# Kernel optimization log

Measured on AMD Instinct MI355X. Metric: run time of the kernel, lower is better.

## Reference

```python
import jax, jax.numpy as jnp
import numpy as np

N_NODES = 100000
N_EDGES = 1600000
D_IN = 128
D_HID = 128
D_OUT = 64


def _glorot(key, shape):
    lim = float(np.sqrt(6.0 / (shape[0] + shape[1])))
    return jax.random.uniform(key, shape, jnp.float32, -lim, lim)


def setup_inputs() -> dict:
    key = jax.random.key(0)
    ks = jax.random.split(key, 8)
    x = jax.random.normal(ks[0], (N_NODES, D_IN), jnp.float32)
    edge_index = jax.random.randint(ks[1], (2, N_EDGES), 0, N_NODES, jnp.int64)
    # SAGEConv layer 0: in=128 -> out=128 (lin_l with bias on aggregated, lin_r no bias on root)
    W_l0 = _glorot(ks[2], (D_IN, D_HID))
    b_l0 = jnp.zeros((D_HID,), jnp.float32)
    W_r0 = _glorot(ks[3], (D_IN, D_HID))
    # SAGEConv layer 1: in=128 -> out=64
    W_l1 = _glorot(ks[4], (D_HID, D_OUT))
    b_l1 = jnp.zeros((D_OUT,), jnp.float32)
    W_r1 = _glorot(ks[5], (D_HID, D_OUT))
    return {"x": x, "edge_index": edge_index,
            "W_l0": W_l0, "b_l0": b_l0, "W_r0": W_r0,
            "W_l1": W_l1, "b_l1": b_l1, "W_r1": W_r1}


def _sage_conv(x, src, dst, W_l, b_l, W_r):
    # mean aggregation of source features at targets (PyG SAGEConv default aggr='mean')
    msgs = x[src]                                              # [E, d_in] irregular gather
    agg = jax.ops.segment_sum(msgs, dst, num_segments=N_NODES)  # [N, d_in]
    cnt = jax.ops.segment_sum(jnp.ones((src.shape[0],), x.dtype), dst,
                              num_segments=N_NODES)            # [N]
    mean = agg / jnp.maximum(cnt, 1.0)[:, None]
    return mean @ W_l + b_l + x @ W_r


def reference(x, edge_index, W_l0, b_l0, W_r0, W_l1, b_l1, W_r1):
    src, dst = edge_index[0], edge_index[1]
    h = _sage_conv(x, src, dst, W_l0, b_l0, W_r0)
    h = jax.nn.relu(h)
    # dropout is identity at inference (training=False)
    out = _sage_conv(h, src, dst, W_l1, b_l1, W_r1)
    return out
```

## Files before the change

### kernel.cpp

```cpp
#include <hip/hip_runtime.h>
#include <type_traits>

#define NN 100000
#define NE 1600000
#define DF 128
#define NBKT 196
#define BKT_SHIFT 9
#define EPB 6250
#define NPB2 391

typedef unsigned short ushort_t;
typedef unsigned int uint_t;
typedef __bf16 bf16x8 __attribute__((ext_vector_type(8)));
typedef float f32x4 __attribute__((ext_vector_type(4)));

union ABFrag { uint4 u; bf16x8 v; ushort_t s[8]; };

__device__ __forceinline__ ushort_t f2bf(float f) {
    uint_t u;
    __builtin_memcpy(&u, &f, 4);
    uint_t rounding = 0x7FFFu + ((u >> 16) & 1u);
    u += rounding;
    return (ushort_t)(u >> 16);
}
__device__ __forceinline__ float lo_f(uint_t u) { return __uint_as_float(u << 16); }
__device__ __forceinline__ float hi_f(uint_t u) { return __uint_as_float(u & 0xffff0000u); }
__device__ __forceinline__ uint_t pack2(float a, float b) {
    return (uint_t)f2bf(a) | ((uint_t)f2bf(b) << 16);
}

__device__ __forceinline__ int detect64(const int* ei, int* s64) {
    if (threadIdx.x < 64) {
        int v = ei[threadIdx.x];
        bool ok = ((threadIdx.x & 1) == 0) || (v == 0);
        unsigned long long m = __ballot(ok);
        if (threadIdx.x == 0) *s64 = (m == 0xFFFFFFFFFFFFFFFFULL) ? 1 : 0;
    }
    __syncthreads();
    return *s64;
}

__global__ __launch_bounds__(256) void k_bktcnt(const int* __restrict__ ei,
                                                int* __restrict__ M) {
    __shared__ int cnt[NBKT];
    __shared__ int s64;
    int t = threadIdx.x, blk = blockIdx.x;
    int is64 = detect64(ei, &s64);
    for (int i = t; i < NBKT; i += 256) cnt[i] = 0;
    __syncthreads();
    int e0 = blk * EPB;
    if (is64) {
        const long long* p = (const long long*)ei;
        for (int i = t; i < EPB; i += 256) {
            int d = (int)p[(size_t)NE + e0 + i];
            atomicAdd(&cnt[d >> BKT_SHIFT], 1);
        }
    } else {
        for (int i = t; i < EPB; i += 256) {
            int d = ei[NE + e0 + i];
            atomicAdd(&cnt[d >> BKT_SHIFT], 1);
        }
    }
    __syncthreads();
    for (int i = t; i < NBKT; i += 256) M[i * 256 + blk] = cnt[i];
}

__global__ __launch_bounds__(256) void k_colscan(int* __restrict__ M, int* __restrict__ colsum) {
    __shared__ int sm[256];
    int t = threadIdx.x, b = blockIdx.x;
    int v = M[b * 256 + t];
    sm[t] = v;
    __syncthreads();
    for (int o = 1; o < 256; o <<= 1) {
        int add = (t >= o) ? sm[t - o] : 0;
        __syncthreads();
        sm[t] += add;
        __syncthreads();
    }
    M[b * 256 + t] = sm[t] - v;
    if (t == 255) colsum[b] = sm[255];
}

__global__ __launch_bounds__(256) void k_bktscan(const int* __restrict__ colsum,
                                                 int* __restrict__ bkbase, int* __restrict__ rs) {
    __shared__ int sm[256];
    int t = threadIdx.x;
    int v = (t < NBKT) ? colsum[t] : 0;
    sm[t] = v;
    __syncthreads();
    for (int o = 1; o < 256; o <<= 1) {
        int add = (t >= o) ? sm[t - o] : 0;
        __syncthreads();
        sm[t] += add;
        __syncthreads();
    }
    if (t <= NBKT) bkbase[t] = sm[t] - v;
    if (t == 0) rs[NN] = NE;
}

__global__ void k_scan512(const int* __restrict__ c2, int* __restrict__ dbase) {
    __shared__ int sm[512];
    int t = threadIdx.x;
    int v = c2[t];
    sm[t] = v;
    __syncthreads();
    for (int o = 1; o < 512; o <<= 1) {
        int add = (t >= o) ? sm[t - o] : 0;
        __syncthreads();
        sm[t] += add;
        __syncthreads();
    }
    dbase[t] = sm[t] - v;
}

__global__ __launch_bounds__(256) void k_bktscatter(const int* __restrict__ ei,
                                                    const int* __restrict__ M,
                                                    const int* __restrict__ bkbase,
                                                    uint2* __restrict__ tmp) {
    __shared__ int cur[NBKT];
    __shared__ int s64;
    int t = threadIdx.x, blk = blockIdx.x;
    int is64 = detect64(ei, &s64);
    for (int i = t; i < NBKT; i += 256) cur[i] = bkbase[i] + M[i * 256 + blk];
    __syncthreads();
    int e0 = blk * EPB;
    if (is64) {
        const long long* p = (const long long*)ei;
        for (int i = t; i < EPB; i += 256) {
            int e = e0 + i;
            int s = (int)p[e], d = (int)p[(size_t)NE + e];
            int pos = atomicAdd(&cur[d >> BKT_SHIFT], 1);
            tmp[pos] = make_uint2((uint_t)s, (uint_t)d);
        }
    } else {
        for (int i = t; i < EPB; i += 256) {
            int e = e0 + i;
            int s = ei[e], d = ei[NE + e];
            int pos = atomicAdd(&cur[d >> BKT_SHIFT], 1);
            tmp[pos] = make_uint2((uint_t)s, (uint_t)d);
        }
    }
}

__global__ __launch_bounds__(256) void k_bktsort(const uint2* __restrict__ tmp,
                                                 const int* __restrict__ bkbase,
                                                 int* __restrict__ rs, int* __restrict__ esrc) {
    __shared__ int hist[512];
    __shared__ int curp[512];
    int t = threadIdx.x, b = blockIdx.x;
    int nbase = b << BKT_SHIFT;
    int bb = bkbase[b], be = bkbase[b + 1];
    hist[t] = 0;
    hist[t + 256] = 0;
    __syncthreads();
    for (int i = bb + t; i < be; i += 256)
        atomicAdd(&hist[(int)tmp[i].y - nbase], 1);
    __syncthreads();
    int ov0 = hist[t], ov1 = hist[t + 256];
    for (int o = 1; o < 512; o <<= 1) {
        int v0 = (t >= o) ? hist[t - o] : 0;
        int v1 = (t + 256 >= o) ? hist[t + 256 - o] : 0;
        __syncthreads();
        hist[t] += v0;
        hist[t + 256] += v1;
        __syncthreads();
    }
    int ex0 = bb + hist[t] - ov0;
    int ex1 = bb + hist[t + 256] - ov1;
    int n0 = nbase + t, n1 = nbase + t + 256;
    if (n0 < NN) rs[n0] = ex0;
    if (n1 < NN) rs[n1] = ex1;
    curp[t] = ex0;
    curp[t + 256] = ex1;
    __syncthreads();
    for (int i = bb + t; i < be; i += 256) {
        uint2 pr = tmp[i];
        int pos = atomicAdd(&curp[(int)pr.y - nbase], 1);
        esrc[pos] = (int)pr.x;
    }
}

__global__ __launch_bounds__(256) void k_dcnt(const int* __restrict__ rs, int* __restrict__ M2) {
    __shared__ int cnt[512];
    int t = threadIdx.x, b = blockIdx.x;
    cnt[t] = 0;
    cnt[t + 256] = 0;
    __syncthreads();
    int base = b * NPB2;
    for (int i = t; i < NPB2; i += 256) {
        int n = base + i;
        if (n < NN) {
            int d = rs[n + 1] - rs[n];
            if (d > 511) d = 511;
            atomicAdd(&cnt[d], 1);
        }
    }
    __syncthreads();
    M2[t * 256 + b] = cnt[t];
    M2[(t + 256) * 256 + b] = cnt[t + 256];
}

__global__ __launch_bounds__(256) void k_dperm(const int* __restrict__ rs,
                                               const int* __restrict__ M2,
                                               const int* __restrict__ dbase,
                                               int* __restrict__ perm) {
    __shared__ int cur[512];
    int t = threadIdx.x, b = blockIdx.x;
    cur[t] = dbase[t] + M2[t * 256 + b];
    cur[t + 256] = dbase[t + 256] + M2[(t + 256) * 256 + b];
    __syncthreads();
    int base = b * NPB2;
    for (int i = t; i < NPB2; i += 256) {
        int n = base + i;
        if (n < NN) {
            int d = rs[n + 1] - rs[n];
            if (d > 511) d = 511;
            int pos = atomicAdd(&cur[d], 1);
            perm[pos] = n;
        }
    }
}

#define CAST_B 12501
__global__ void k_prep(const float* __restrict__ x, ushort_t* __restrict__ xb,
                       const float* __restrict__ Wl0, const float* __restrict__ Wr0,
                       ushort_t* __restrict__ pw0,
                       const float* __restrict__ Wl1, const float* __restrict__ Wr1,
                       ushort_t* __restrict__ pw1) {
    const int n4 = NN * DF / 4;
    int blk = blockIdx.x, t = threadIdx.x;
    if (blk < CAST_B) {
        int i = blk * 256 + t;
        if (i < n4) {
            float4 f = ((const float4*)x)[i];
            uint2 o;
            o.x = pack2(f.x, f.y);
            o.y = pack2(f.z, f.w);
            ((uint2*)xb)[i] = o;
        } else if (i < n4 + 32) {
            ((uint2*)xb)[i] = make_uint2(0u, 0u);
        }
    } else if (blk < CAST_B + 128) {
        int idx = (blk - CAST_B) * 256 + t;
        int j = idx & 7;
        int lane = (idx >> 3) & 63;
        int rem = idx / 512;
        int tt = rem % 8;
        int s = rem / 8;
        int quad = lane >> 4, l16 = lane & 15;
        int k = (s & 3) * 32 + quad * 8 + j;
        int n = tt * 16 + l16;
        const float* W = (s < 4) ? Wl0 : Wr0;
        pw0[idx] = f2bf(W[k * 128 + n]);
    } else {
        int idx = (blk - CAST_B - 128) * 256 + t;
        int j = idx & 7;
        int lane = (idx >> 3) & 63;
        int rem = idx / 512;
        int tt = rem % 8;
        int s = rem / 8;
        int quad = lane >> 4, l16 = lane & 15;
        int k = s * 32 + quad * 8 + j;
        int n = (tt & 3) * 16 + l16;
        const float* W = (tt < 4) ? Wl1 : Wr1;
        pw1[idx] = f2bf(W[k * 64 + n]);
    }
}

__global__ __launch_bounds__(256) void k_agg0(const ushort_t* __restrict__ xb,
                                              const int* __restrict__ rs,
                                              const int* __restrict__ esrc,
                                              const int* __restrict__ perm,
                                              ushort_t* __restrict__ outm) {
    int wv = threadIdx.x >> 6;
    int lane = threadIdx.x & 63;
    int l16 = lane & 15, gbase = lane & 48;
    int slot = (blockIdx.x * 4 + wv) * 4 + (lane >> 4);
    int n = perm[slot];
    int s0 = rs[n];
    int deg = rs[n + 1] - s0;
    if (deg == 0) s0 = 0;
    int md = deg;
    md = max(md, __shfl_xor(md, 16));
    md = max(md, __shfl_xor(md, 32));
    float acc[8] = {0.f, 0.f, 0.f, 0.f, 0.f, 0.f, 0.f, 0.f};
    const ushort_t* fb = xb + l16 * 8;
    int clampIdx = (deg > 0) ? deg - 1 : 0;
    for (int c = 0; c < md; c += 16) {
        int ii = c + l16;
        if (ii > clampIdx) ii = clampIdx;
        int my = esrc[s0 + ii];
        int lim = md - c;
        if (lim > 16) lim = 16;
        int e = 0;
        for (; e + 4 <= lim; e += 4) {
            int r0 = __shfl(my, gbase + e);
            int r1 = __shfl(my, gbase + e + 1);
            int r2 = __shfl(my, gbase + e + 2);
            int r3 = __shfl(my, gbase + e + 3);
            r0 = (c + e < deg) ? r0 : NN;
            r1 = (c + e + 1 < deg) ? r1 : NN;
            r2 = (c + e + 2 < deg) ? r2 : NN;
            r3 = (c + e + 3 < deg) ? r3 : NN;
            uint4 v0 = *(const uint4*)(fb + (size_t)r0 * DF);
            uint4 v1 = *(const uint4*)(fb + (size_t)r1 * DF);
            uint4 v2 = *(const uint4*)(fb + (size_t)r2 * DF);
            uint4 v3 = *(const uint4*)(fb + (size_t)r3 * DF);
            acc[0] += lo_f(v0.x); acc[1] += hi_f(v0.x); acc[2] += lo_f(v0.y); acc[3] += hi_f(v0.y);
            acc[4] += lo_f(v0.z); acc[5] += hi_f(v0.z); acc[6] += lo_f(v0.w); acc[7] += hi_f(v0.w);
            acc[0] += lo_f(v1.x); acc[1] += hi_f(v1.x); acc[2] += lo_f(v1.y); acc[3] += hi_f(v1.y);
            acc[4] += lo_f(v1.z); acc[5] += hi_f(v1.z); acc[6] += lo_f(v1.w); acc[7] += hi_f(v1.w);
            acc[0] += lo_f(v2.x); acc[1] += hi_f(v2.x); acc[2] += lo_f(v2.y); acc[3] += hi_f(v2.y);
            acc[4] += lo_f(v2.z); acc[5] += hi_f(v2.z); acc[6] += lo_f(v2.w); acc[7] += hi_f(v2.w);
            acc[0] += lo_f(v3.x); acc[1] += hi_f(v3.x); acc[2] += lo_f(v3.y); acc[3] += hi_f(v3.y);
            acc[4] += lo_f(v3.z); acc[5] += hi_f(v3.z); acc[6] += lo_f(v3.w); acc[7] += hi_f(v3.w);
        }
        for (; e < lim; ++e) {
            int r = __shfl(my, gbase + e);
            r = (c + e < deg) ? r : NN;
            uint4 v = *(const uint4*)(fb + (size_t)r * DF);
            acc[0] += lo_f(v.x); acc[1] += hi_f(v.x); acc[2] += lo_f(v.y); acc[3] += hi_f(v.y);
            acc[4] += lo_f(v.z); acc[5] += hi_f(v.z); acc[6] += lo_f(v.w); acc[7] += hi_f(v.w);
        }
    }
    float inv = 1.0f / (float)(deg > 0 ? deg : 1);
    uint4 o;
    o.x = pack2(acc[0] * inv, acc[1] * inv);
    o.y = pack2(acc[2] * inv, acc[3] * inv);
    o.z = pack2(acc[4] * inv, acc[5] * inv);
    o.w = pack2(acc[6] * inv, acc[7] * inv);
    *(uint4*)(outm + (size_t)n * DF + l16 * 8) = o;
}

__global__ __launch_bounds__(256) void k_gemmF(const ushort_t* __restrict__ A0,
                                               const ushort_t* __restrict__ A1,
                                               const ushort_t* __restrict__ pw0,
                                               const float* __restrict__ bl0,
                                               const ushort_t* __restrict__ pw1,
                                               const float* __restrict__ bl1,
                                               ushort_t* __restrict__ tbuf,
                                               float* __restrict__ rbuf) {
    __shared__ ushort_t h_lds[64][136];
    int warp = threadIdx.x >> 6;
    int lane = threadIdx.x & 63;
    int quad = lane >> 4;
    int l16 = lane & 15;
    int m0 = blockIdx.x * 64 + warp * 16;

    int rowA = m0 + l16;
    if (rowA >= NN) rowA = NN - 1;
    const int kofs = quad * 8;

    f32x4 acc[8];
#pragma unroll
    for (int t = 0; t < 8; t++) acc[t] = (f32x4){0.f, 0.f, 0.f, 0.f};

#pragma unroll
    for (int s = 0; s < 8; s++) {
        const ushort_t* Ab = (s < 4) ? A0 : A1;
        int kk = (s & 3) * 32 + kofs;
        ABFrag a;
        a.u = *(const uint4*)(Ab + (size_t)rowA * DF + kk);
#pragma unroll
        for (int t = 0; t < 8; t++) {
            ABFrag b;
            b.u = *(const uint4*)(pw0 + ((size_t)(s * 8 + t) * 64 + lane) * 8);
            acc[t] = __builtin_amdgcn_mfma_f32_16x16x32_bf16(a.v, b.v, acc[t], 0, 0, 0);
        }
    }
#pragma unroll
    for (int t = 0; t < 8; t++) {
        int col = t * 16 + l16;
        float bv = bl0[col];
#pragma unroll
        for (int r = 0; r < 4; r++)
            h_lds[warp * 16 + quad * 4 + r][col] = f2bf(fmaxf(acc[t][r] + bv, 0.f));
    }
    __syncthreads();

    f32x4 c1[8];
#pragma unroll
    for (int t = 0; t < 8; t++) c1[t] = (f32x4){0.f, 0.f, 0.f, 0.f};
#pragma unroll
    for (int s = 0; s < 4; s++) {
        ABFrag a;
        a.u = *(const uint4*)&h_lds[warp * 16 + l16][s * 32 + kofs];
#pragma unroll
        for (int t = 0; t < 8; t++) {
            ABFrag b;
            b.u = *(const uint4*)(pw1 + ((size_t)(s * 8 + t) * 64 + lane) * 8);
            c1[t] = __builtin_amdgcn_mfma_f32_16x16x32_bf16(a.v, b.v, c1[t], 0, 0, 0);
        }
    }
#pragma unroll
    for (int t = 0; t < 8; t++) {
        int cc = (t & 3) * 16 + l16;
        if (t < 4) {
#pragma unroll
            for (int r = 0; r < 4; r++) {
                int row = m0 + quad * 4 + r;
                if (row < NN) tbuf[(size_t)row * 64 + cc] = f2bf(c1[t][r]);
            }
        } else {
            float bv = bl1[cc];
#pragma unroll
            for (int r = 0; r < 4; r++) {
                int row = m0 + quad * 4 + r;
                if (row < NN) rbuf[(size_t)row * 64 + cc] = c1[t][r] + bv;
            }
        }
    }
    if (blockIdx.x == 0 && threadIdx.x < 32)
        ((uint_t*)(tbuf + (size_t)NN * 64))[threadIdx.x] = 0u;
}

__global__ __launch_bounds__(256) void k_agg2(const ushort_t* __restrict__ tbuf,
                                              const float* __restrict__ rbuf,
                                              const int* __restrict__ rs,
                                              const int* __restrict__ esrc,
                                              const int* __restrict__ perm,
                                              float* __restrict__ out) {
    int wv = threadIdx.x >> 6;
    int lane = threadIdx.x & 63;
    int li = lane & 7;
    int gbase = lane & 56;
    int slot = (blockIdx.x * 4 + wv) * 8 + (lane >> 3);
    int n = perm[slot];
    int s0 = rs[n];
    int deg = rs[n + 1] - s0;
    if (deg == 0) s0 = 0;
    int md = deg;
    md = max(md, __shfl_xor(md, 8));
    md = max(md, __shfl_xor(md, 16));
    md = max(md, __shfl_xor(md, 32));
    float acc[8] = {0.f, 0.f, 0.f, 0.f, 0.f, 0.f, 0.f, 0.f};
    const ushort_t* fb = tbuf + li * 8;
    int clampIdx = (deg > 0) ? deg - 1 : 0;
    for (int c = 0; c < md; c += 8) {
        int ii = c + li;
        if (ii > clampIdx) ii = clampIdx;
        int my = esrc[s0 + ii];
        int lim = md - c;
        if (lim > 8) lim = 8;
        int e = 0;
        for (; e + 4 <= lim; e += 4) {
            int r0 = __shfl(my, gbase + e);
            int r1 = __shfl(my, gbase + e + 1);
            int r2 = __shfl(my, gbase + e + 2);
            int r3 = __shfl(my, gbase + e + 3);
            r0 = (c + e < deg) ? r0 : NN;
            r1 = (c + e + 1 < deg) ? r1 : NN;
            r2 = (c + e + 2 < deg) ? r2 : NN;
            r3 = (c + e + 3 < deg) ? r3 : NN;
            uint4 v0 = *(const uint4*)(fb + (size_t)r0 * 64);
            uint4 v1 = *(const uint4*)(fb + (size_t)r1 * 64);
            uint4 v2 = *(const uint4*)(fb + (size_t)r2 * 64);
            uint4 v3 = *(const uint4*)(fb + (size_t)r3 * 64);
            acc[0] += lo_f(v0.x); acc[1] += hi_f(v0.x); acc[2] += lo_f(v0.y); acc[3] += hi_f(v0.y);
            acc[4] += lo_f(v0.z); acc[5] += hi_f(v0.z); acc[6] += lo_f(v0.w); acc[7] += hi_f(v0.w);
            acc[0] += lo_f(v1.x); acc[1] += hi_f(v1.x); acc[2] += lo_f(v1.y); acc[3] += hi_f(v1.y);
            acc[4] += lo_f(v1.z); acc[5] += hi_f(v1.z); acc[6] += lo_f(v1.w); acc[7] += hi_f(v1.w);
            acc[0] += lo_f(v2.x); acc[1] += hi_f(v2.x); acc[2] += lo_f(v2.y); acc[3] += hi_f(v2.y);
            acc[4] += lo_f(v2.z); acc[5] += hi_f(v2.z); acc[6] += lo_f(v2.w); acc[7] += hi_f(v2.w);
            acc[0] += lo_f(v3.x); acc[1] += hi_f(v3.x); acc[2] += lo_f(v3.y); acc[3] += hi_f(v3.y);
            acc[4] += lo_f(v3.z); acc[5] += hi_f(v3.z); acc[6] += lo_f(v3.w); acc[7] += hi_f(v3.w);
        }
        for (; e < lim; ++e) {
            int r = __shfl(my, gbase + e);
            r = (c + e < deg) ? r : NN;
            uint4 v = *(const uint4*)(fb + (size_t)r * 64);
            acc[0] += lo_f(v.x); acc[1] += hi_f(v.x); acc[2] += lo_f(v.y); acc[3] += hi_f(v.y);
            acc[4] += lo_f(v.z); acc[5] += hi_f(v.z); acc[6] += lo_f(v.w); acc[7] += hi_f(v.w);
        }
    }
    float inv = 1.0f / (float)(deg > 0 ? deg : 1);
    const float4* rp = (const float4*)(rbuf + (size_t)n * 64 + li * 8);
    float4 ra = rp[0], rb = rp[1];
    float4 oa, ob;
    oa.x = acc[0] * inv + ra.x; oa.y = acc[1] * inv + ra.y;
    oa.z = acc[2] * inv + ra.z; oa.w = acc[3] * inv + ra.w;
    ob.x = acc[4] * inv + rb.x; ob.y = acc[5] * inv + rb.y;
    ob.z = acc[6] * inv + rb.z; ob.w = acc[7] * inv + rb.w;
    float4* op = (float4*)(out + (size_t)n * 64 + li * 8);
    op[0] = oa;
    op[1] = ob;
}

extern "C" void kernel_launch(void* const* d_in, const int* in_sizes, int n_in,
                              void* d_out, int out_size, void* d_ws, size_t ws_size,
                              hipStream_t stream) {
    const float* x   = (const float*)d_in[0];
    const int*   ei  = (const int*)d_in[1];
    const float* Wl0 = (const float*)d_in[2];
    const float* bl0 = (const float*)d_in[3];
    const float* Wr0 = (const float*)d_in[4];
    const float* Wl1 = (const float*)d_in[5];
    const float* bl1 = (const float*)d_in[6];
    const float* Wr1 = (const float*)d_in[7];
    float* out = (float*)d_out;

    char* ws = (char*)d_ws;
    size_t off = 0;
    auto alloc = [&](size_t b) {
        size_t o = off;
        off += (b + 255) & ~(size_t)255;
        return o;
    };
    int* rs      = (int*)(ws + alloc((size_t)(NN + 1) * 4));
    int* M       = (int*)(ws + alloc((size_t)NBKT * 256 * 4));
    int* colsum  = (int*)(ws + alloc((size_t)NBKT * 4));
    int* bkbase  = (int*)(ws + alloc((size_t)(NBKT + 1) * 4));
    int* M2      = (int*)(ws + alloc((size_t)512 * 256 * 4));
    int* colsum2 = (int*)(ws + alloc((size_t)512 * 4));
    int* dbase   = (int*)(ws + alloc((size_t)512 * 4));
    int* perm    = (int*)(ws + alloc((size_t)NN * 4));
    int* esrc    = (int*)(ws + alloc((size_t)NE * 4));
    ushort_t* pw0  = (ushort_t*)(ws + alloc((size_t)8 * 8 * 512 * 2));
    ushort_t* pw1  = (ushort_t*)(ws + alloc((size_t)4 * 8 * 512 * 2));
    ushort_t* xb   = (ushort_t*)(ws + alloc((size_t)(NN + 1) * DF * 2));
    ushort_t* mean = (ushort_t*)(ws + alloc((size_t)NN * DF * 2));
    ushort_t* tbuf = (ushort_t*)(ws + alloc((size_t)(NN + 1) * 64 * 2));
    float*    rbuf = (float*)(ws + alloc((size_t)NN * 64 * 4));
    uint2* tmp = (uint2*)mean;

    k_bktcnt<<<256, 256, 0, stream>>>(ei, M);
    k_colscan<<<NBKT, 256, 0, stream>>>(M, colsum);
    k_bktscan<<<1, 256, 0, stream>>>(colsum, bkbase, rs);
    k_bktscatter<<<256, 256, 0, stream>>>(ei, M, bkbase, tmp);
    k_bktsort<<<NBKT, 256, 0, stream>>>(tmp, bkbase, rs, esrc);
    k_dcnt<<<256, 256, 0, stream>>>(rs, M2);
    k_colscan<<<512, 256, 0, stream>>>(M2, colsum2);
    k_scan512<<<1, 512, 0, stream>>>(colsum2, dbase);
    k_dperm<<<256, 256, 0, stream>>>(rs, M2, dbase, perm);
    k_prep<<<CAST_B + 128 + 64, 256, 0, stream>>>(x, xb, Wl0, Wr0, pw0, Wl1, Wr1, pw1);

    k_agg0<<<NN / 16, 256, 0, stream>>>(xb, rs, esrc, perm, mean);
    k_gemmF<<<(NN + 63) / 64, 256, 0, stream>>>(mean, xb, pw0, bl0, pw1, bl1, tbuf, rbuf);
    k_agg2<<<NN / 32, 256, 0, stream>>>(tbuf, rbuf, rs, esrc, perm, out);
}
```

Baseline: 316.2 us.

## Gather x in FP8, pack bucket edges, drop degree sort and bf16 root copy

Casts x to FP8 for the first-layer neighbor gather, which halves the bytes each gathered row reads. The root GEMM term now reads fp32 x directly and converts it to bf16 in registers. Bucket-scatter edges are packed into one 32-bit word (17-bit source, 9-bit local destination) instead of a uint2. The degree-sorted node permutation and its four kernels are removed, so aggregation walks nodes in natural order. The FP8 gather reduces accuracy, and removing the permutation may worsen load balance across waves.

New measurement: 273.6 us. -13.5%, faster.

```diff
diff --git a/kernel.cpp b/kernel.cpp
--- a/kernel.cpp
+++ b/kernel.cpp
@@ -7,12 +7,13 @@
 #define NBKT 196
 #define BKT_SHIFT 9
 #define EPB 6250
-#define NPB2 391
 
 typedef unsigned short ushort_t;
 typedef unsigned int uint_t;
+typedef unsigned char uchar_t;
 typedef __bf16 bf16x8 __attribute__((ext_vector_type(8)));
 typedef float f32x4 __attribute__((ext_vector_type(4)));
+typedef float f32x2 __attribute__((ext_vector_type(2)));
 
 union ABFrag { uint4 u; bf16x8 v; ushort_t s[8]; };
 
@@ -98,25 +99,10 @@
     if (t == 0) rs[NN] = NE;
 }
 
-__global__ void k_scan512(const int* __restrict__ c2, int* __restrict__ dbase) {
-    __shared__ int sm[512];
-    int t = threadIdx.x;
-    int v = c2[t];
-    sm[t] = v;
-    __syncthreads();
-    for (int o = 1; o < 512; o <<= 1) {
-        int add = (t >= o) ? sm[t - o] : 0;
-        __syncthreads();
-        sm[t] += add;
-        __syncthreads();
-    }
-    dbase[t] = sm[t] - v;
-}
-
 __global__ __launch_bounds__(256) void k_bktscatter(const int* __restrict__ ei,
                                                     const int* __restrict__ M,
                                                     const int* __restrict__ bkbase,
-                                                    uint2* __restrict__ tmp) {
+                                                    uint_t* __restrict__ tmp) {
     __shared__ int cur[NBKT];
     __shared__ int s64;
     int t = threadIdx.x, blk = blockIdx.x;
@@ -130,19 +116,19 @@
             int e = e0 + i;
             int s = (int)p[e], d = (int)p[(size_t)NE + e];
             int pos = atomicAdd(&cur[d >> BKT_SHIFT], 1);
-            tmp[pos] = make_uint2((uint_t)s, (uint_t)d);
+            tmp[pos] = (uint_t)s | ((uint_t)(d & 511) << 17);
         }
     } else {
         for (int i = t; i < EPB; i += 256) {
             int e = e0 + i;
             int s = ei[e], d = ei[NE + e];
             int pos = atomicAdd(&cur[d >> BKT_SHIFT], 1);
-            tmp[pos] = make_uint2((uint_t)s, (uint_t)d);
-        }
-    }
-}
-
-__global__ __launch_bounds__(256) void k_bktsort(const uint2* __restrict__ tmp,
+            tmp[pos] = (uint_t)s | ((uint_t)(d & 511) << 17);
+        }
+    }
+}
+
+__global__ __launch_bounds__(256) void k_bktsort(const uint_t* __restrict__ tmp,
                                                  const int* __restrict__ bkbase,
                                                  int* __restrict__ rs, int* __restrict__ esrc) {
     __shared__ int hist[512];
@@ -154,7 +140,7 @@
     hist[t + 256] = 0;
     __syncthreads();
     for (int i = bb + t; i < be; i += 256)
-        atomicAdd(&hist[(int)tmp[i].y - nbase], 1);
+        atomicAdd(&hist[tmp[i] >> 17], 1);
     __syncthreads();
     int ov0 = hist[t], ov1 = hist[t + 256];
     for (int o = 1; o < 512; o <<= 1) {
@@ -174,55 +160,14 @@
     curp[t + 256] = ex1;
     __syncthreads();
     for (int i = bb + t; i < be; i += 256) {
-        uint2 pr = tmp[i];
-        int pos = atomicAdd(&curp[(int)pr.y - nbase], 1);
-        esrc[pos] = (int)pr.x;
-    }
-}
-
-__global__ __launch_bounds__(256) void k_dcnt(const int* __restrict__ rs, int* __restrict__ M2) {
-    __shared__ int cnt[512];
-    int t = threadIdx.x, b = blockIdx.x;
-    cnt[t] = 0;
-    cnt[t + 256] = 0;
-    __syncthreads();
-    int base = b * NPB2;
-    for (int i = t; i < NPB2; i += 256) {
-        int n = base + i;
-        if (n < NN) {
-            int d = rs[n + 1] - rs[n];
-            if (d > 511) d = 511;
-            atomicAdd(&cnt[d], 1);
-        }
-    }
-    __syncthreads();
-    M2[t * 256 + b] = cnt[t];
-    M2[(t + 256) * 256 + b] = cnt[t + 256];
-}
-
-__global__ __launch_bounds__(256) void k_dperm(const int* __restrict__ rs,
-                                               const int* __restrict__ M2,
-                                               const int* __restrict__ dbase,
-                                               int* __restrict__ perm) {
-    __shared__ int cur[512];
-    int t = threadIdx.x, b = blockIdx.x;
-    cur[t] = dbase[t] + M2[t * 256 + b];
-    cur[t + 256] = dbase[t + 256] + M2[(t + 256) * 256 + b];
-    __syncthreads();
-    int base = b * NPB2;
-    for (int i = t; i < NPB2; i += 256) {
-        int n = base + i;
-        if (n < NN) {
-            int d = rs[n + 1] - rs[n];
-            if (d > 511) d = 511;
-            int pos = atomicAdd(&cur[d], 1);
-            perm[pos] = n;
-        }
+        uint_t pk = tmp[i];
+        int pos = atomicAdd(&curp[pk >> 17], 1);
+        esrc[pos] = (int)(pk & 0x1FFFFu);
     }
 }
 
 #define CAST_B 12501
-__global__ void k_prep(const float* __restrict__ x, ushort_t* __restrict__ xb,
+__global__ void k_prep(const float* __restrict__ x, uchar_t* __restrict__ x8,
                        const float* __restrict__ Wl0, const float* __restrict__ Wr0,
                        ushort_t* __restrict__ pw0,
                        const float* __restrict__ Wl1, const float* __restrict__ Wr1,
@@ -233,12 +178,11 @@
         int i = blk * 256 + t;
         if (i < n4) {
             float4 f = ((const float4*)x)[i];
-            uint2 o;
-            o.x = pack2(f.x, f.y);
-            o.y = pack2(f.z, f.w);
-            ((uint2*)xb)[i] = o;
+            int lo = __builtin_amdgcn_cvt_pk_fp8_f32(f.x, f.y, 0, false);
+            int u = __builtin_amdgcn_cvt_pk_fp8_f32(f.z, f.w, lo, true);
+            ((uint_t*)x8)[i] = (uint_t)u;
         } else if (i < n4 + 32) {
-            ((uint2*)xb)[i] = make_uint2(0u, 0u);
+            ((uint_t*)x8)[i] = 0u;
         }
     } else if (blk < CAST_B + 128) {
         int idx = (blk - CAST_B) * 256 + t;
@@ -267,16 +211,14 @@
     }
 }
 
-__global__ __launch_bounds__(256) void k_agg0(const ushort_t* __restrict__ xb,
+__global__ __launch_bounds__(256) void k_agg0(const uchar_t* __restrict__ x8,
                                               const int* __restrict__ rs,
                                               const int* __restrict__ esrc,
-                                              const int* __restrict__ perm,
                                               ushort_t* __restrict__ outm) {
     int wv = threadIdx.x >> 6;
     int lane = threadIdx.x & 63;
     int l16 = lane & 15, gbase = lane & 48;
-    int slot = (blockIdx.x * 4 + wv) * 4 + (lane >> 4);
-    int n = perm[slot];
+    int n = (blockIdx.x * 4 + wv) * 4 + (lane >> 4);
     int s0 = rs[n];
     int deg = rs[n + 1] - s0;
     if (deg == 0) s0 = 0;
@@ -284,7 +226,7 @@
     md = max(md, __shfl_xor(md, 16));
     md = max(md, __shfl_xor(md, 32));
     float acc[8] = {0.f, 0.f, 0.f, 0.f, 0.f, 0.f, 0.f, 0.f};
-    const ushort_t* fb = xb + l16 * 8;
+    const uchar_t* fb = x8 + l16 * 8;
     int clampIdx = (deg > 0) ? deg - 1 : 0;
     for (int c = 0; c < md; c += 16) {
         int ii = c + l16;
@@ -302,25 +244,31 @@
             r1 = (c + e + 1 < deg) ? r1 : NN;
             r2 = (c + e + 2 < deg) ? r2 : NN;
             r3 = (c + e + 3 < deg) ? r3 : NN;
-            uint4 v0 = *(const uint4*)(fb + (size_t)r0 * DF);
-            uint4 v1 = *(const uint4*)(fb + (size_t)r1 * DF);
-            uint4 v2 = *(const uint4*)(fb + (size_t)r2 * DF);
-            uint4 v3 = *(const uint4*)(fb + (size_t)r3 * DF);
-            acc[0] += lo_f(v0.x); acc[1] += hi_f(v0.x); acc[2] += lo_f(v0.y); acc[3] += hi_f(v0.y);
-            acc[4] += lo_f(v0.z); acc[5] += hi_f(v0.z); acc[6] += lo_f(v0.w); acc[7] += hi_f(v0.w);
-            acc[0] += lo_f(v1.x); acc[1] += hi_f(v1.x); acc[2] += lo_f(v1.y); acc[3] += hi_f(v1.y);
-            acc[4] += lo_f(v1.z); acc[5] += hi_f(v1.z); acc[6] += lo_f(v1.w); acc[7] += hi_f(v1.w);
-            acc[0] += lo_f(v2.x); acc[1] += hi_f(v2.x); acc[2] += lo_f(v2.y); acc[3] += hi_f(v2.y);
-            acc[4] += lo_f(v2.z); acc[5] += hi_f(v2.z); acc[6] += lo_f(v2.w); acc[7] += hi_f(v2.w);
-            acc[0] += lo_f(v3.x); acc[1] += hi_f(v3.x); acc[2] += lo_f(v3.y); acc[3] += hi_f(v3.y);
-            acc[4] += lo_f(v3.z); acc[5] += hi_f(v3.z); acc[6] += lo_f(v3.w); acc[7] += hi_f(v3.w);
+            uint2 v0 = *(const uint2*)(fb + (size_t)r0 * DF);
+            uint2 v1 = *(const uint2*)(fb + (size_t)r1 * DF);
+            uint2 v2 = *(const uint2*)(fb + (size_t)r2 * DF);
+            uint2 v3 = *(const uint2*)(fb + (size_t)r3 * DF);
+#pragma unroll
+            for (int q = 0; q < 4; q++) {
+                uint2 v = (q == 0) ? v0 : (q == 1) ? v1 : (q == 2) ? v2 : v3;
+                f32x2 p0 = __builtin_amdgcn_cvt_pk_f32_fp8(v.x, false);
+                f32x2 p1 = __builtin_amdgcn_cvt_pk_f32_fp8(v.x, true);
+                f32x2 p2 = __builtin_amdgcn_cvt_pk_f32_fp8(v.y, false);
+                f32x2 p3 = __builtin_amdgcn_cvt_pk_f32_fp8(v.y, true);
+                acc[0] += p0.x; acc[1] += p0.y; acc[2] += p1.x; acc[3] += p1.y;
+                acc[4] += p2.x; acc[5] += p2.y; acc[6] += p3.x; acc[7] += p3.y;
+            }
         }
         for (; e < lim; ++e) {
             int r = __shfl(my, gbase + e);
             r = (c + e < deg) ? r : NN;
-            uint4 v = *(const uint4*)(fb + (size_t)r * DF);
-            acc[0] += lo_f(v.x); acc[1] += hi_f(v.x); acc[2] += lo_f(v.y); acc[3] += hi_f(v.y);
-            acc[4] += lo_f(v.z); acc[5] += hi_f(v.z); acc[6] += lo_f(v.w); acc[7] += hi_f(v.w);
+            uint2 v = *(const uint2*)(fb + (size_t)r * DF);
+            f32x2 p0 = __builtin_amdgcn_cvt_pk_f32_fp8(v.x, false);
+            f32x2 p1 = __builtin_amdgcn_cvt_pk_f32_fp8(v.x, true);
+            f32x2 p2 = __builtin_amdgcn_cvt_pk_f32_fp8(v.y, false);
+            f32x2 p3 = __builtin_amdgcn_cvt_pk_f32_fp8(v.y, true);
+            acc[0] += p0.x; acc[1] += p0.y; acc[2] += p1.x; acc[3] += p1.y;
+            acc[4] += p2.x; acc[5] += p2.y; acc[6] += p3.x; acc[7] += p3.y;
         }
     }
     float inv = 1.0f / (float)(deg > 0 ? deg : 1);
@@ -333,7 +281,7 @@
 }
 
 __global__ __launch_bounds__(256) void k_gemmF(const ushort_t* __restrict__ A0,
-                                               const ushort_t* __restrict__ A1,
+                                               const float* __restrict__ x,
                                                const ushort_t* __restrict__ pw0,
                                                const float* __restrict__ bl0,
                                                const ushort_t* __restrict__ pw1,
@@ -357,10 +305,19 @@
 
 #pragma unroll
     for (int s = 0; s < 8; s++) {
-        const ushort_t* Ab = (s < 4) ? A0 : A1;
         int kk = (s & 3) * 32 + kofs;
         ABFrag a;
-        a.u = *(const uint4*)(Ab + (size_t)rowA * DF + kk);
+        if (s < 4) {
+            a.u = *(const uint4*)(A0 + (size_t)rowA * DF + kk);
+        } else {
+            const float* xr = x + (size_t)rowA * DF + kk;
+            float4 fa = *(const float4*)xr;
+            float4 fc = *(const float4*)(xr + 4);
+            a.u.x = pack2(fa.x, fa.y);
+            a.u.y = pack2(fa.z, fa.w);
+            a.u.z = pack2(fc.x, fc.y);
+            a.u.w = pack2(fc.z, fc.w);
+        }
 #pragma unroll
         for (int t = 0; t < 8; t++) {
             ABFrag b;
@@ -418,14 +375,12 @@
                                               const float* __restrict__ rbuf,
                                               const int* __restrict__ rs,
                                               const int* __restrict__ esrc,
-                                              const int* __restrict__ perm,
                                               float* __restrict__ out) {
     int wv = threadIdx.x >> 6;
     int lane = threadIdx.x & 63;
     int li = lane & 7;
     int gbase = lane & 56;
-    int slot = (blockIdx.x * 4 + wv) * 8 + (lane >> 3);
-    int n = perm[slot];
+    int n = (blockIdx.x * 4 + wv) * 8 + (lane >> 3);
     int s0 = rs[n];
     int deg = rs[n + 1] - s0;
     if (deg == 0) s0 = 0;
@@ -506,35 +461,27 @@
         off += (b + 255) & ~(size_t)255;
         return o;
     };
-    int* rs      = (int*)(ws + alloc((size_t)(NN + 1) * 4));
-    int* M       = (int*)(ws + alloc((size_t)NBKT * 256 * 4));
-    int* colsum  = (int*)(ws + alloc((size_t)NBKT * 4));
-    int* bkbase  = (int*)(ws + alloc((size_t)(NBKT + 1) * 4));
-    int* M2      = (int*)(ws + alloc((size_t)512 * 256 * 4));
-    int* colsum2 = (int*)(ws + alloc((size_t)512 * 4));
-    int* dbase   = (int*)(ws + alloc((size_t)512 * 4));
-    int* perm    = (int*)(ws + alloc((size_t)NN * 4));
-    int* esrc    = (int*)(ws + alloc((size_t)NE * 4));
+    int* rs     = (int*)(ws + alloc((size_t)(NN + 1) * 4));
+    int* M      = (int*)(ws + alloc((size_t)NBKT * 256 * 4));
+    int* colsum = (int*)(ws + alloc((size_t)NBKT * 4));
+    int* bkbase = (int*)(ws + alloc((size_t)(NBKT + 1) * 4));
+    int* esrc   = (int*)(ws + alloc((size_t)NE * 4));
     ushort_t* pw0  = (ushort_t*)(ws + alloc((size_t)8 * 8 * 512 * 2));
     ushort_t* pw1  = (ushort_t*)(ws + alloc((size_t)4 * 8 * 512 * 2));
-    ushort_t* xb   = (ushort_t*)(ws + alloc((size_t)(NN + 1) * DF * 2));
+    uchar_t*  x8   = (uchar_t*)(ws + alloc((size_t)(NN + 1) * DF));
     ushort_t* mean = (ushort_t*)(ws + alloc((size_t)NN * DF * 2));
     ushort_t* tbuf = (ushort_t*)(ws + alloc((size_t)(NN + 1) * 64 * 2));
     float*    rbuf = (float*)(ws + alloc((size_t)NN * 64 * 4));
-    uint2* tmp = (uint2*)mean;
+    uint_t* tmp = (uint_t*)mean;
 
     k_bktcnt<<<256, 256, 0, stream>>>(ei, M);
     k_colscan<<<NBKT, 256, 0, stream>>>(M, colsum);
     k_bktscan<<<1, 256, 0, stream>>>(colsum, bkbase, rs);
     k_bktscatter<<<256, 256, 0, stream>>>(ei, M, bkbase, tmp);
     k_bktsort<<<NBKT, 256, 0, stream>>>(tmp, bkbase, rs, esrc);
-    k_dcnt<<<256, 256, 0, stream>>>(rs, M2);
-    k_colscan<<<512, 256, 0, stream>>>(M2, colsum2);
-    k_scan512<<<1, 512, 0, stream>>>(colsum2, dbase);
-    k_dperm<<<256, 256, 0, stream>>>(rs, M2, dbase, perm);
-    k_prep<<<CAST_B + 128 + 64, 256, 0, stream>>>(x, xb, Wl0, Wr0, pw0, Wl1, Wr1, pw1);
-
-    k_agg0<<<NN / 16, 256, 0, stream>>>(xb, rs, esrc, perm, mean);
-    k_gemmF<<<(NN + 63) / 64, 256, 0, stream>>>(mean, xb, pw0, bl0, pw1, bl1, tbuf, rbuf);
-    k_agg2<<<NN / 32, 256, 0, stream>>>(tbuf, rbuf, rs, esrc, perm, out);
-}
+    k_prep<<<CAST_B + 128 + 64, 256, 0, stream>>>(x, x8, Wl0, Wr0, pw0, Wl1, Wr1, pw1);
+
+    k_agg0<<<NN / 16, 256, 0, stream>>>(x8, rs, esrc, mean);
+    k_gemmF<<<(NN + 63) / 64, 256, 0, stream>>>(mean, x, pw0, bl0, pw1, bl1, tbuf, rbuf);
+    k_agg2<<<NN / 32, 256, 0, stream>>>(tbuf, rbuf, rs, esrc, out);
+}
```
